# Optimization experiments

Measured on AMD Instinct MI355X. Metric: run time of the kernel, lower is better.

Reference implementation:

```python
import jax, jax.numpy as jnp
import numpy as np

CUR, FULL, BS, DIM, H, D = 512, 1024, 4, 1024, 16, 64
PREV = FULL - CUR


def _rel_shift(x):
    # x: (cur, full, bs, h) -- TransformerXL relative shift (pad/reshape/slice)
    cur, full = x.shape[0], x.shape[1]
    zero_pad = jnp.zeros((cur, 1) + x.shape[2:], x.dtype)
    x_padded = jnp.concatenate([zero_pad, x], axis=1)           # (cur, full+1, bs, h)
    x_padded = x_padded.reshape((full + 1, cur) + x.shape[2:])  # view trick
    x = x_padded[1:].reshape(x.shape)
    tri = jnp.tril(jnp.ones((cur, full), x.dtype), full - cur)  # keep valid band
    return x * tri[:, :, None, None]


def setup_inputs() -> dict:
    key = jax.random.key(0)
    ks = jax.random.split(key, 12)
    s = jnp.float32(0.02)
    # causal mask: query i (at absolute pos i+PREV) may not attend to key j > i+PREV
    mask = (jnp.arange(FULL)[None, :] > (jnp.arange(CUR)[:, None] + PREV))[:, :, None]
    return {
        "inputs": jax.random.normal(ks[0], (CUR, BS, DIM), jnp.float32),
        "pos_embedding": jax.random.normal(ks[1], (FULL, 1, DIM), jnp.float32),
        "full_input": jax.random.normal(ks[2], (FULL, BS, DIM), jnp.float32),
        "u": jax.random.normal(ks[3], (H, D), jnp.float32) * s,
        "v": jax.random.normal(ks[4], (H, D), jnp.float32) * s,
        "W_kv": jax.random.normal(ks[5], (DIM, 2 * H * D), jnp.float32) * s,
        "b_kv": jnp.zeros((2 * H * D,), jnp.float32),
        "W_q": jax.random.normal(ks[6], (DIM, H * D), jnp.float32) * s,
        "b_q": jnp.zeros((H * D,), jnp.float32),
        "W_pos": jax.random.normal(ks[7], (DIM, H * D), jnp.float32) * s,
        "b_pos": jnp.zeros((H * D,), jnp.float32),
        "W_proj": jax.random.normal(ks[8], (H * D, DIM), jnp.float32) * s,
        "b_proj": jnp.zeros((DIM,), jnp.float32),
        "mask": mask,
    }


def reference(inputs, pos_embedding, full_input, u, v, W_kv, b_kv, W_q, b_q,
              W_pos, b_pos, W_proj, b_proj, mask):
    cur_seq, bs = inputs.shape[0], inputs.shape[1]
    full_seq = full_input.shape[0]
    scale = jnp.float32(1.0 / D ** 0.5)

    kv = full_input @ W_kv + b_kv                       # (full, bs, 2*H*D)
    key, value = jnp.split(kv, 2, axis=-1)
    query = inputs @ W_q + b_q                          # (cur, bs, H*D)
    r = (pos_embedding @ W_pos + b_pos).reshape(full_seq, H, D)

    key = key.reshape(full_seq, bs, H, D)
    value = value.reshape(full_seq, bs, H, D)
    query = query.reshape(cur_seq, bs, H, D)

    content_attn = jnp.einsum('ibhd,jbhd->ijbh', query + u, key)
    position_attn = jnp.einsum('ibhd,jhd->ijbh', query + v, r)
    position_attn = _rel_shift(position_attn)

    attn = (content_attn + position_attn) * scale       # (cur, full, bs, h)
    attn = jnp.where(mask[:, :, :, None], -jnp.inf, attn)
    attn = jax.nn.softmax(attn, axis=1)                 # softmax over full_seq

    attn_vec = jnp.einsum('ijbh,jbhd->ibhd', attn, value)
    attn_vec = attn_vec.reshape(cur_seq, bs, H * D)
    return attn_vec @ W_proj + b_proj                   # (cur, bs, DIM)
```

## Files before the change

### kernel.cpp

```cpp
#include <hip/hip_runtime.h>


typedef unsigned short u16;
typedef short short8 __attribute__((ext_vector_type(8)));
typedef float f32x4 __attribute__((ext_vector_type(4)));

#define BSZ 4
#define PREV 512

__device__ __forceinline__ float b2f(u16 u) {
  union { unsigned int i; float f; } x; x.i = ((unsigned int)u) << 16; return x.f;
}
__device__ __forceinline__ u16 f2b(float f) {
  union { float f; unsigned int i; } x; x.f = f;
  unsigned int u = x.i;
  return (u16)((u + 0x7fffu + ((u >> 16) & 1u)) >> 16);
}
__device__ __forceinline__ void storeC(u16* C, size_t idx, float v) { C[idx] = f2b(v); }
__device__ __forceinline__ void storeC(float* C, size_t idx, float v) { C[idx] = v; }

__device__ __forceinline__ void load_lds16(const u16* g, void* l) {
  __builtin_amdgcn_global_load_lds(
      (const __attribute__((address_space(1))) unsigned int*)g,
      (__attribute__((address_space(3))) unsigned int*)l, 16, 0, 0);
}

__device__ __forceinline__ size_t pidx8(int row, int k, int K32) {
  return (((size_t)((row >> 4) * K32 + (k >> 5))) << 9) +
         (((k >> 3) & 3) << 7) + ((row & 15) << 3);
}

__global__ __launch_bounds__(256)
void prep(const float* __restrict__ s0, const float* __restrict__ s1,
          const float* __restrict__ s2, u16* __restrict__ d0,
          u16* __restrict__ d1, u16* __restrict__ d2,
          const float* __restrict__ W0, const float* __restrict__ W1,
          const float* __restrict__ W2, const float* __restrict__ W3,
          u16* __restrict__ T0, u16* __restrict__ T1,
          u16* __restrict__ T2, u16* __restrict__ T3) {
  __shared__ u16 ld[64 * 66];
  const int bxg = blockIdx.x;
  if (bxg < 3584) {
    const float* s; u16* d; size_t base;
    if (bxg < 2048)      { s = s0; d = d0; base = (size_t)bxg * 2048; }
    else if (bxg < 3072) { s = s1; d = d1; base = (size_t)(bxg - 2048) * 2048; }
    else                 { s = s2; d = d2; base = (size_t)(bxg - 3072) * 2048; }
    size_t i = base + (size_t)threadIdx.x * 8;
    const f32x4* p = reinterpret_cast<const f32x4*>(s + i);
    f32x4 a = p[0], b = p[1];
    short8 r;
#pragma unroll
    for (int e = 0; e < 4; e++) { r[e] = (short)f2b(a[e]); r[e + 4] = (short)f2b(b[e]); }
    int row = (int)(i >> 10), k = (int)(i & 1023);
    *reinterpret_cast<short8*>(d + pidx8(row, k, 32)) = r;
    return;
  }
  const int l = bxg - 3584;
  const int z = l >> 9;
  const int rem = l & 511;
  const int bx = rem & 31, by = rem >> 5;
  const float* W; u16* T; int N;
  if (z == 0)      { W = W0; T = T0; N = 2048; }
  else if (z == 1) { W = W1; T = T1; N = 1024; }
  else if (z == 2) { W = W2; T = T2; N = 1024; }
  else             { W = W3; T = T3; N = 1024; }
  const int n0 = bx * 64, k0 = by * 64;
  if (n0 >= N) return;

  const int tid = threadIdx.x;
#pragma unroll
  for (int rep = 0; rep < 16; rep++) {
    int idx = tid + 256 * rep;
    int kk = idx >> 6, nn = idx & 63;
    ld[kk * 66 + nn] = f2b(W[(size_t)(k0 + kk) * N + n0 + nn]);
  }
  __syncthreads();
#pragma unroll
  for (int rep = 0; rep < 2; rep++) {
    int idx = tid + 256 * rep;
    int nn = idx >> 3, k8 = (idx & 7) * 8;
    short8 r;
#pragma unroll
    for (int e = 0; e < 8; e++) r[e] = (short)ld[(k8 + e) * 66 + nn];
    *reinterpret_cast<short8*>(T + pidx8(n0 + nn, k0 + k8, 32)) = r;
  }
}

template <typename OT, int MODE>
__device__ __forceinline__ void gemm_core(
    short* __restrict__ at, short* __restrict__ bt,
    const u16* __restrict__ A, const u16* __restrict__ BT,
    const float* __restrict__ bias, OT* __restrict__ C, u16* __restrict__ C2,
    int N, int K, int bx, int by)
{
  const int tid = threadIdx.x;
  const int lane = tid & 63, w = tid >> 6;
  const int wr = w >> 1, wc = w & 1;
  const int quad = lane >> 4, ml = lane & 15;
  const int row0 = by * 128, col0 = bx * 128;
  const int K32 = K >> 5;

  f32x4 acc[4][4];
  const f32x4 fzero = {0.f, 0.f, 0.f, 0.f};
#pragma unroll
  for (int i = 0; i < 4; i++)
#pragma unroll
    for (int j = 0; j < 4; j++) acc[i][j] = fzero;

  for (int k0 = 0; k0 < K; k0 += 64) {
    __syncthreads();
#pragma unroll
    for (int i = 0; i < 4; i++) {
      int c = 4 * w + i;
      int mc = c >> 1, kc = c & 1;
      size_t ca = ((size_t)(((row0 >> 4) + mc) * K32 + (k0 >> 5) + kc)) << 9;
      size_t cb = ((size_t)(((col0 >> 4) + mc) * K32 + (k0 >> 5) + kc)) << 9;
      load_lds16(A + ca + lane * 8, (void*)(at + c * 512));
      load_lds16(BT + cb + lane * 8, (void*)(bt + c * 512));
    }
    __syncthreads();

    short8 af[4][2], bf[4][2];
#pragma unroll
    for (int mc = 0; mc < 4; mc++)
#pragma unroll
      for (int kc = 0; kc < 2; kc++)
        af[mc][kc] = *reinterpret_cast<const short8*>(at + ((((wr * 4 + mc) * 2 + kc) * 64) + lane) * 8);
#pragma unroll
    for (int nc = 0; nc < 4; nc++)
#pragma unroll
      for (int kc = 0; kc < 2; kc++)
        bf[nc][kc] = *reinterpret_cast<const short8*>(bt + ((((wc * 4 + nc) * 2 + kc) * 64) + lane) * 8);

#pragma unroll
    for (int mc = 0; mc < 4; mc++)
#pragma unroll
      for (int nc = 0; nc < 4; nc++)
#pragma unroll
        for (int kc = 0; kc < 2; kc++)
          acc[mc][nc] = __builtin_amdgcn_mfma_f32_16x16x32_bf16(af[mc][kc], bf[nc][kc], acc[mc][nc], 0, 0, 0);
  }

#pragma unroll
  for (int nc = 0; nc < 4; nc++) {
    int col = col0 + wc * 64 + nc * 16 + ml;
    float bv = bias[col];
#pragma unroll
    for (int mc = 0; mc < 4; mc++) {
#pragma unroll
      for (int reg = 0; reg < 4; reg++) {
        int row = row0 + wr * 64 + mc * 16 + quad * 4 + reg;
        float val = acc[mc][nc][reg] + bv;
        if constexpr (MODE == 0) {
          storeC(C, (size_t)row * N + col, val);
        } else if constexpr (MODE == 1) {
          int j = row >> 2, bb = row & 3;
          int tile = j >> 6, jl = j & 63;
          if (col < 1024) {
            int h = col >> 6, d = col & 63;
            int ncj = jl >> 4, nlj = jl & 15, kcd = d >> 5, qdd = (d >> 3) & 3, jjd = d & 7;
            C[((size_t)(bb * 16 + h) * 16 + tile) * 4096 +
              ((ncj * 2 + kcd) * 64 + qdd * 16 + nlj) * 8 + jjd] = f2b(val);
          } else {
            int c2 = col - 1024;
            int h = c2 >> 6, d = c2 & 63;
            int ncd = d >> 4, nld = d & 15, kcj = jl >> 5, qdj = (jl >> 3) & 3, jjj = jl & 7;
            C2[((size_t)(bb * 16 + h) * 16 + tile) * 4096 +
               ((kcj * 4 + ncd) * 64 + qdj * 16 + nld) * 8 + jjj] = f2b(val);
          }
        } else {
          int h = col >> 6, d = col & 63;
          C[((size_t)h * 1024 + row) * 64 + d] = f2b(val);
        }
      }
    }
  }
}

__global__ __launch_bounds__(256, 2)
void gemm3(const u16* __restrict__ fibf, const u16* __restrict__ WkvT,
           const float* __restrict__ b_kv, u16* __restrict__ Kt2, u16* __restrict__ Vt2,
           const u16* __restrict__ inbf, const u16* __restrict__ WqT,
           const float* __restrict__ b_q, u16* __restrict__ qq,
           const u16* __restrict__ pebf, const u16* __restrict__ WposT,
           const float* __restrict__ b_pos, u16* __restrict__ Rt)
{
  __shared__ __align__(16) short at[8192];
  __shared__ __align__(16) short bt[8192];
  const int id = blockIdx.x;
  if (id < 512) {
    gemm_core<u16, 1>(at, bt, fibf, WkvT, b_kv, Kt2, Vt2, 2048, 1024, id & 15, id >> 4);
  } else if (id < 640) {
    const int l = id - 512;
    gemm_core<u16, 0>(at, bt, inbf, WqT, b_q, qq, (u16*)nullptr, 1024, 1024, l & 7, l >> 3);
  } else {
    const int l = id - 640;
    gemm_core<u16, 2>(at, bt, pebf, WposT, b_pos, Rt, (u16*)nullptr, 1024, 1024, l & 7, l >> 3);
  }
}

__global__ __launch_bounds__(256, 2)
void gemm_proj(const u16* __restrict__ A, const u16* __restrict__ BT,
               const float* __restrict__ bias, float* __restrict__ C)
{
  __shared__ __align__(16) short at[8192];
  __shared__ __align__(16) short bt[8192];
  gemm_core<float, 0>(at, bt, A, BT, bias, C, (u16*)nullptr, 1024, 1024,
                      blockIdx.x, blockIdx.y);
}

__global__ __launch_bounds__(256, 4)
void flash_xl(const u16* __restrict__ q, const u16* __restrict__ Kt2,
              const u16* __restrict__ Vt2, const u16* __restrict__ Rt,
              const float* __restrict__ u, const float* __restrict__ v,
              float* __restrict__ po, float* __restrict__ pm,
              float* __restrict__ pl)
{
  __shared__ __align__(16) short kb[4096];
  __shared__ __align__(16) short vb[4096];
  __shared__ __align__(16) short pt[4][1024];

  const int tid = threadIdx.x, lane = tid & 63, w = tid >> 6;
  const int quad = lane >> 4, ml = lane & 15;
  const int x = blockIdx.x;
  int it, s, nseg;
  if (x < 12) { int g = x / 3; it = 7 - g; s = x - g * 3; nseg = 3; }
  else        { int y = x - 12; it = 3 - (y >> 1); s = y & 1; nseg = 2; }
  const int nt = it + 9;
  const int qn = (nseg == 3) ? (nt / 3) : (nt >> 1);
  const int rn = nt - qn * nseg;
  const int ts = s * qn + (s < rn ? s : rn);
  const int te = ts + qn + (s < rn ? 1 : 0);

  const int b = blockIdx.y, h = blockIdx.z;
  const int bh = b * 16 + h;
  const int i0 = it * 64, ig0 = i0 + w * 16;

  const u16* Kbase = Kt2 + ((size_t)(b * 16 + h) * 16) * 4096;
  const u16* Vbase = Vt2 + ((size_t)(b * 16 + h) * 16) * 4096;
  const u16* Rp = Rt + (size_t)h * 65536;

  short8 qu[2], qvf[2];
  {
    int ig = ig0 + ml;
#pragma unroll
    for (int kc = 0; kc < 2; kc++) {
      int dbase = kc * 32 + quad * 8;
      short8 qq = *reinterpret_cast<const short8*>(q + ((size_t)ig * BSZ + b) * 1024 + h * 64 + dbase);
      const f32x4* up = reinterpret_cast<const f32x4*>(u + h * 64 + dbase);
      const f32x4* vp = reinterpret_cast<const f32x4*>(v + h * 64 + dbase);
      f32x4 u0 = up[0], u1 = up[1], v0 = vp[0], v1 = vp[1];
#pragma unroll
      for (int e = 0; e < 8; e++) {
        float qf = b2f((u16)qq[e]);
        float uu = (e < 4) ? u0[e] : u1[e - 4];
        float vv = (e < 4) ? v0[e] : v1[e - 4];
        qu[kc][e]  = (short)f2b((qf + uu) * 0.125f);
        qvf[kc][e] = (short)f2b((qf + vv) * 0.125f);
      }
    }
  }

  const f32x4 fzero = {0.f, 0.f, 0.f, 0.f};
  f32x4 o_acc[4];
#pragma unroll
  for (int i = 0; i < 4; i++) o_acc[i] = fzero;
  float m_run[4], l_run[4];
#pragma unroll
  for (int i = 0; i < 4; i++) { m_run[i] = -1e30f; l_run[i] = 0.f; }

  short8 pk0, pk1, pv0, pv1;
  {
    const u16* kg = Kbase + (size_t)ts * 4096;
    const u16* vg = Vbase + (size_t)ts * 4096;
    pk0 = *reinterpret_cast<const short8*>(kg + tid * 8);
    pk1 = *reinterpret_cast<const short8*>(kg + 2048 + tid * 8);
    pv0 = *reinterpret_cast<const short8*>(vg + tid * 8);
    pv1 = *reinterpret_cast<const short8*>(vg + 2048 + tid * 8);
  }

  for (int t = ts; t < te; t++) {
    const int j0 = t * 64;
    __syncthreads();
    *reinterpret_cast<short8*>(kb + tid * 8) = pk0;
    *reinterpret_cast<short8*>(kb + 2048 + tid * 8) = pk1;
    *reinterpret_cast<short8*>(vb + tid * 8) = pv0;
    *reinterpret_cast<short8*>(vb + 2048 + tid * 8) = pv1;
    __syncthreads();

    if (t + 1 < te) {
      const u16* kg = Kbase + (size_t)(t + 1) * 4096;
      const u16* vg = Vbase + (size_t)(t + 1) * 4096;
      pk0 = *reinterpret_cast<const short8*>(kg + tid * 8);
      pk1 = *reinterpret_cast<const short8*>(kg + 2048 + tid * 8);
      pv0 = *reinterpret_cast<const short8*>(vg + tid * 8);
      pv1 = *reinterpret_cast<const short8*>(vg + 2048 + tid * 8);
    }

    f32x4 sc[4];
#pragma unroll
    for (int nc = 0; nc < 4; nc++) {
      sc[nc] = fzero;
#pragma unroll
      for (int kc = 0; kc < 2; kc++) {
        short8 kf = *reinterpret_cast<const short8*>(kb + ((nc * 2 + kc) * 64 + lane) * 8);
        sc[nc] = __builtin_amdgcn_mfma_f32_16x16x32_bf16(qu[kc], kf, sc[nc], 0, 0, 0);
      }
    }
    const int relstart = j0 - ig0 + 496;
    f32x4 p2[5];
#pragma unroll
    for (int c = 0; c < 5; c++) {
      p2[c] = fzero;
      int rel = relstart + c * 16 + ml;
      if (rel > 1023) rel = 1023;
      const u16* rp = Rp + (size_t)rel * 64 + quad * 8;
#pragma unroll
      for (int kc = 0; kc < 2; kc++) {
        short8 rf = *reinterpret_cast<const short8*>(rp + kc * 32);
        p2[c] = __builtin_amdgcn_mfma_f32_16x16x32_bf16(qvf[kc], rf, p2[c], 0, 0, 0);
      }
    }

    const bool anymask = (j0 + 63) > (ig0 + PREV);
    float pv_[4][4];
    float tmax[4] = {-1e30f, -1e30f, -1e30f, -1e30f};
#pragma unroll
    for (int reg = 0; reg < 4; reg++) {
      int rowl = quad * 4 + reg;
      int src = quad * 16 + ((ml - rowl - 1) & 15);
      bool hi = ml > rowl;
      float sh[5];
#pragma unroll
      for (int c = 0; c < 5; c++) sh[c] = __shfl(p2[c][reg], src, 64);
#pragma unroll
      for (int nc = 0; nc < 4; nc++) {
        float sv = sc[nc][reg] + (hi ? sh[nc + 1] : sh[nc]);
        if (anymask) {
          int jg = j0 + nc * 16 + ml;
          if (jg > ig0 + rowl + PREV) sv = -1e30f;
        }
        pv_[nc][reg] = sv;
        tmax[reg] = fmaxf(tmax[reg], sv);
      }
    }
#pragma unroll
    for (int reg = 0; reg < 4; reg++) {
      float tm = tmax[reg];
#pragma unroll
      for (int off = 1; off < 16; off <<= 1) tm = fmaxf(tm, __shfl_xor(tm, off, 64));
      float mnew = fmaxf(m_run[reg], tm);
      float alpha = __expf(m_run[reg] - mnew);
      float rs = 0.f;
#pragma unroll
      for (int nc = 0; nc < 4; nc++) {
        float p = __expf(pv_[nc][reg] - mnew);
        pv_[nc][reg] = p;
        rs += p;
      }
#pragma unroll
      for (int off = 1; off < 16; off <<= 1) rs += __shfl_xor(rs, off, 64);
      l_run[reg] = l_run[reg] * alpha + rs;
      m_run[reg] = mnew;
#pragma unroll
      for (int nc = 0; nc < 4; nc++) o_acc[nc][reg] *= alpha;
    }

#pragma unroll
    for (int nc = 0; nc < 4; nc++) {
      int jl = nc * 16 + ml;
      int kc = nc >> 1, qdj = (jl >> 3) & 3, jj = ml & 7;
#pragma unroll
      for (int reg = 0; reg < 4; reg++) {
        int rowl = quad * 4 + reg;
        pt[w][(kc * 64 + qdj * 16 + rowl) * 8 + jj] = (short)f2b(pv_[nc][reg]);
      }
    }
    short8 pf[2];
    pf[0] = *reinterpret_cast<const short8*>(pt[w] + (0 * 64 + lane) * 8);
    pf[1] = *reinterpret_cast<const short8*>(pt[w] + (1 * 64 + lane) * 8);

#pragma unroll
    for (int ncd = 0; ncd < 4; ncd++)
#pragma unroll
      for (int kc = 0; kc < 2; kc++) {
        short8 vf = *reinterpret_cast<const short8*>(vb + ((kc * 4 + ncd) * 64 + lane) * 8);
        o_acc[ncd] = __builtin_amdgcn_mfma_f32_16x16x32_bf16(pf[kc], vf, o_acc[ncd], 0, 0, 0);
      }
  }

#pragma unroll
  for (int reg = 0; reg < 4; reg++) {
    int ig = ig0 + quad * 4 + reg;
    size_t ridx = (s < 2) ? ((size_t)(s * 512 + ig) * 64 + bh)
                          : ((size_t)65536 + (size_t)(ig - 256) * 64 + bh);
    if (ml == 0) { pm[ridx] = m_run[reg]; pl[ridx] = l_run[reg]; }
#pragma unroll
    for (int ncd = 0; ncd < 4; ncd++)
      po[ridx * 64 + ncd * 16 + ml] = o_acc[ncd][reg];
  }
}

__global__ __launch_bounds__(256)
void combine(const float* __restrict__ po, const float* __restrict__ pm,
             const float* __restrict__ pl, u16* __restrict__ av) {
  int t = blockIdx.x * 256 + threadIdx.x;
  int r0 = t >> 3, d8 = (t & 7) * 8;
  int ig = r0 >> 6, b = (r0 >> 4) & 3, h = r0 & 15;
  float m1 = pm[r0], m2 = pm[32768 + r0];
  float l1 = pl[r0], l2 = pl[32768 + r0];
  const f32x4* p1 = reinterpret_cast<const f32x4*>(po + (size_t)r0 * 64 + d8);
  const f32x4* p2 = reinterpret_cast<const f32x4*>(po + ((size_t)32768 + r0) * 64 + d8);
  f32x4 o1a = p1[0], o1b = p1[1], o2a = p2[0], o2b = p2[1];
  float m = fmaxf(m1, m2);
  const bool h3 = ig >= 256;
  int r2 = r0 + 49152;
  float m3 = -1e30f, l3 = 0.f;
  f32x4 o3a = {0.f, 0.f, 0.f, 0.f}, o3b = {0.f, 0.f, 0.f, 0.f};
  if (h3) {
    m3 = pm[r2]; l3 = pl[r2];
    const f32x4* p3 = reinterpret_cast<const f32x4*>(po + (size_t)r2 * 64 + d8);
    o3a = p3[0]; o3b = p3[1];
    m = fmaxf(m, m3);
  }
  float a1 = __expf(m1 - m), a2 = __expf(m2 - m);
  float a3 = h3 ? __expf(m3 - m) : 0.f;
  float l = l1 * a1 + l2 * a2 + l3 * a3;
  short8 r;
#pragma unroll
  for (int e = 0; e < 4; e++) {
    r[e]     = (short)f2b((o1a[e] * a1 + o2a[e] * a2 + o3a[e] * a3) / l);
    r[e + 4] = (short)f2b((o1b[e] * a1 + o2b[e] * a2 + o3b[e] * a3) / l);
  }
  int row = ig * 4 + b, k = h * 64 + d8;
  *reinterpret_cast<short8*>(av + pidx8(row, k, 32)) = r;
}

extern "C" void kernel_launch(void* const* d_in, const int* in_sizes, int n_in,
                              void* d_out, int out_size, void* d_ws, size_t ws_size,
                              hipStream_t stream) {
  (void)in_sizes; (void)n_in; (void)out_size; (void)ws_size;

  const float* inputs  = (const float*)d_in[0];
  const float* pos_emb = (const float*)d_in[1];
  const float* full_in = (const float*)d_in[2];
  const float* u       = (const float*)d_in[3];
  const float* v       = (const float*)d_in[4];
  const float* W_kv    = (const float*)d_in[5];
  const float* b_kv    = (const float*)d_in[6];
  const float* W_q     = (const float*)d_in[7];
  const float* b_q     = (const float*)d_in[8];
  const float* W_pos   = (const float*)d_in[9];
  const float* b_pos   = (const float*)d_in[10];
  const float* W_proj  = (const float*)d_in[11];
  const float* b_proj  = (const float*)d_in[12];
  float* out = (float*)d_out;

  char* ws = (char*)d_ws;
  u16* Kt2   = (u16*)(ws);
  u16* Vt2   = (u16*)(ws + ( 8u << 20));
  u16* qq    = (u16*)(ws + (16u << 20));
  u16* Rt    = (u16*)(ws + (20u << 20));
  u16* av    = (u16*)(ws + (22u << 20));
  u16* WkvT  = (u16*)(ws + (26u << 20));
  u16* WqT   = (u16*)(ws + (30u << 20));
  u16* WposT = (u16*)(ws + (32u << 20));
  u16* WprojT= (u16*)(ws + (34u << 20));
  u16* fibf  = (u16*)(ws + (36u << 20));
  u16* inbf  = (u16*)(ws + (44u << 20));
  u16* pebf  = (u16*)(ws + (48u << 20));
  float* po  = (float*)(ws + (36u << 20));
  float* pm  = (float*)(ws + (56u << 20));
  float* pl  = (float*)(ws + (57u << 20));

  hipLaunchKernelGGL(prep, dim3(5632), dim3(256), 0, stream,
                     full_in, inputs, pos_emb, fibf, inbf, pebf,
                     W_kv, W_q, W_pos, W_proj, WkvT, WqT, WposT, WprojT);

  hipLaunchKernelGGL(gemm3, dim3(704), dim3(256), 0, stream,
                     fibf, WkvT, b_kv, Kt2, Vt2,
                     inbf, WqT, b_q, qq,
                     pebf, WposT, b_pos, Rt);

  hipLaunchKernelGGL(flash_xl, dim3(20, 4, 16), dim3(256), 0, stream,
                     qq, Kt2, Vt2, Rt, u, v, po, pm, pl);
  hipLaunchKernelGGL(combine, dim3(1024), dim3(256), 0, stream, po, pm, pl, av);

  hipLaunchKernelGGL(gemm_proj, dim3(8, 16), dim3(256), 0, stream,
                     av, WprojT, b_proj, out);
}
```

Before: 231.5 us.

## Split every query tile into two KV segments and compute row sums via MFMA

Replaces the uneven 3-way/2-way KV split with a uniform 2-way split across all 8 query tiles, shrinking the grid from 20 to 16 x-blocks and removing the third partial from the combine kernel and the workspace. The softmax row sum is no longer computed with exp accumulation plus shuffle reductions. It now comes from an extra pair of MFMAs that multiply the bf16 probability tile by a ones vector. This cuts shuffle and ALU work in the inner loop but sums bf16-rounded probabilities rather than fp32 ones. The coarser split may also leave long tiles less balanced.

```diff
diff --git a/kernel.cpp b/kernel.cpp
--- a/kernel.cpp
+++ b/kernel.cpp
@@ -223,14 +223,10 @@
   const int tid = threadIdx.x, lane = tid & 63, w = tid >> 6;
   const int quad = lane >> 4, ml = lane & 15;
   const int x = blockIdx.x;
-  int it, s, nseg;
-  if (x < 12) { int g = x / 3; it = 7 - g; s = x - g * 3; nseg = 3; }
-  else        { int y = x - 12; it = 3 - (y >> 1); s = y & 1; nseg = 2; }
+  const int it = 7 - (x >> 1), s = x & 1;
   const int nt = it + 9;
-  const int qn = (nseg == 3) ? (nt / 3) : (nt >> 1);
-  const int rn = nt - qn * nseg;
-  const int ts = s * qn + (s < rn ? s : rn);
-  const int te = ts + qn + (s < rn ? 1 : 0);
+  const int nt0 = (nt + 1) >> 1;
+  const int ts = s ? nt0 : 0, te = s ? nt : nt0;
 
   const int b = blockIdx.y, h = blockIdx.z;
   const int bh = b * 16 + h;
@@ -260,6 +256,10 @@
       }
     }
   }
+
+  short8 kones;
+#pragma unroll
+  for (int e = 0; e < 8; e++) kones[e] = (short)0x3F80;
 
   const f32x4 fzero = {0.f, 0.f, 0.f, 0.f};
   f32x4 o_acc[4];
@@ -351,16 +351,10 @@
       for (int off = 1; off < 16; off <<= 1) tm = fmaxf(tm, __shfl_xor(tm, off, 64));
       float mnew = fmaxf(m_run[reg], tm);
       float alpha = __expf(m_run[reg] - mnew);
-      float rs = 0.f;
-#pragma unroll
-      for (int nc = 0; nc < 4; nc++) {
-        float p = __expf(pv_[nc][reg] - mnew);
-        pv_[nc][reg] = p;
-        rs += p;
-      }
-#pragma unroll
-      for (int off = 1; off < 16; off <<= 1) rs += __shfl_xor(rs, off, 64);
-      l_run[reg] = l_run[reg] * alpha + rs;
+#pragma unroll
+      for (int nc = 0; nc < 4; nc++)
+        pv_[nc][reg] = __expf(pv_[nc][reg] - mnew);
+      l_run[reg] *= alpha;
       m_run[reg] = mnew;
 #pragma unroll
       for (int nc = 0; nc < 4; nc++) o_acc[nc][reg] *= alpha;
@@ -380,6 +374,10 @@
     pf[0] = *reinterpret_cast<const short8*>(pt[w] + (0 * 64 + lane) * 8);
     pf[1] = *reinterpret_cast<const short8*>(pt[w] + (1 * 64 + lane) * 8);
 
+    f32x4 lsum = fzero;
+    lsum = __builtin_amdgcn_mfma_f32_16x16x32_bf16(pf[0], kones, lsum, 0, 0, 0);
+    lsum = __builtin_amdgcn_mfma_f32_16x16x32_bf16(pf[1], kones, lsum, 0, 0, 0);
+
 #pragma unroll
     for (int ncd = 0; ncd < 4; ncd++)
 #pragma unroll
@@ -387,13 +385,14 @@
         short8 vf = *reinterpret_cast<const short8*>(vb + ((kc * 4 + ncd) * 64 + lane) * 8);
         o_acc[ncd] = __builtin_amdgcn_mfma_f32_16x16x32_bf16(pf[kc], vf, o_acc[ncd], 0, 0, 0);
       }
+#pragma unroll
+    for (int reg = 0; reg < 4; reg++) l_run[reg] += lsum[reg];
   }
 
 #pragma unroll
   for (int reg = 0; reg < 4; reg++) {
     int ig = ig0 + quad * 4 + reg;
-    size_t ridx = (s < 2) ? ((size_t)(s * 512 + ig) * 64 + bh)
-                          : ((size_t)65536 + (size_t)(ig - 256) * 64 + bh);
+    size_t ridx = (size_t)(s * 512 + ig) * 64 + bh;
     if (ml == 0) { pm[ridx] = m_run[reg]; pl[ridx] = l_run[reg]; }
 #pragma unroll
     for (int ncd = 0; ncd < 4; ncd++)
@@ -413,24 +412,13 @@
   const f32x4* p2 = reinterpret_cast<const f32x4*>(po + ((size_t)32768 + r0) * 64 + d8);
   f32x4 o1a = p1[0], o1b = p1[1], o2a = p2[0], o2b = p2[1];
   float m = fmaxf(m1, m2);
-  const bool h3 = ig >= 256;
-  int r2 = r0 + 49152;
-  float m3 = -1e30f, l3 = 0.f;
-  f32x4 o3a = {0.f, 0.f, 0.f, 0.f}, o3b = {0.f, 0.f, 0.f, 0.f};
-  if (h3) {
-    m3 = pm[r2]; l3 = pl[r2];
-    const f32x4* p3 = reinterpret_cast<const f32x4*>(po + (size_t)r2 * 64 + d8);
-    o3a = p3[0]; o3b = p3[1];
-    m = fmaxf(m, m3);
-  }
   float a1 = __expf(m1 - m), a2 = __expf(m2 - m);
-  float a3 = h3 ? __expf(m3 - m) : 0.f;
-  float l = l1 * a1 + l2 * a2 + l3 * a3;
+  float l = l1 * a1 + l2 * a2;
   short8 r;
 #pragma unroll
   for (int e = 0; e < 4; e++) {
-    r[e]     = (short)f2b((o1a[e] * a1 + o2a[e] * a2 + o3a[e] * a3) / l);
-    r[e + 4] = (short)f2b((o1b[e] * a1 + o2b[e] * a2 + o3b[e] * a3) / l);
+    r[e]     = (short)f2b((o1a[e] * a1 + o2a[e] * a2) / l);
+    r[e + 4] = (short)f2b((o1b[e] * a1 + o2b[e] * a2) / l);
   }
   int row = ig * 4 + b, k = h * 64 + d8;
   *reinterpret_cast<short8*>(av + pidx8(row, k, 32)) = r;
@@ -470,8 +458,8 @@
   u16* inbf  = (u16*)(ws + (44u << 20));
   u16* pebf  = (u16*)(ws + (48u << 20));
   float* po  = (float*)(ws + (36u << 20));
-  float* pm  = (float*)(ws + (56u << 20));
-  float* pl  = (float*)(ws + (57u << 20));
+  float* pm  = (float*)(ws + (52u << 20));
+  float* pl  = (float*)(ws + (52u << 20) + (256u << 10));
 
   hipLaunchKernelGGL(prep, dim3(5632), dim3(256), 0, stream,
                      full_in, inputs, pos_emb, fibf, inbf, pebf,
@@ -482,7 +470,7 @@
                      inbf, WqT, b_q, qq,
                      pebf, WposT, b_pos, Rt);
 
-  hipLaunchKernelGGL(flash_xl, dim3(20, 4, 16), dim3(256), 0, stream,
+  hipLaunchKernelGGL(flash_xl, dim3(16, 4, 16), dim3(256), 0, stream,
                      qq, Kt2, Vt2, Rt, u, v, po, pm, pl);
   hipLaunchKernelGGL(combine, dim3(1024), dim3(256), 0, stream, po, pm, pl, av);
 
```

New measurement: 223.1 us. 3.6% less time.
